# Optimization experiments

Measured on AMD Instinct MI355X. Metric: run time of the kernel, lower is better.

## Reference

```python
import jax, jax.numpy as jnp
import numpy as np

EPS = 1e-5
DG = 8          # deformable groups
KK = 9          # 3x3 taps


def group_norm(x, w, b, G=32, eps=EPS):
    B, C, H, W = x.shape
    xr = x.reshape(B, G, -1)
    m = xr.mean(-1, keepdims=True)
    v = xr.var(-1, keepdims=True)
    xn = ((xr - m) * jax.lax.rsqrt(v + eps)).reshape(B, C, H, W)
    return xn * w[None, :, None, None] + b[None, :, None, None]


def conv1x1(x, w, b):
    return jnp.einsum('bchw,oc->bohw', x, w[:, :, 0, 0]) + b[None, :, None, None]


def conv3x3(x, w, b):
    y = jax.lax.conv_general_dilated(x, w, (1, 1), ((1, 1), (1, 1)),
                                     dimension_numbers=('NCHW', 'OIHW', 'NCHW'))
    return y + b[None, :, None, None]


def bilinear_resize(x, Ho, Wo):
    # matches F.interpolate(mode='bilinear', align_corners=False)
    B, C, H, W = x.shape
    sy = jnp.maximum((jnp.arange(Ho, dtype=x.dtype) + 0.5) * (H / Ho) - 0.5, 0.0)
    sx = jnp.maximum((jnp.arange(Wo, dtype=x.dtype) + 0.5) * (W / Wo) - 0.5, 0.0)
    y0 = jnp.floor(sy).astype(jnp.int32); y1 = jnp.minimum(y0 + 1, H - 1)
    x0 = jnp.floor(sx).astype(jnp.int32); x1 = jnp.minimum(x0 + 1, W - 1)
    fy = (sy - y0)[None, None, :, None]
    fx = (sx - x0)[None, None, None, :]
    v00 = x[:, :, y0][:, :, :, x0]; v01 = x[:, :, y0][:, :, :, x1]
    v10 = x[:, :, y1][:, :, :, x0]; v11 = x[:, :, y1][:, :, :, x1]
    return (v00 * (1 - fy) * (1 - fx) + v01 * (1 - fy) * fx
            + v10 * fy * (1 - fx) + v11 * fy * fx)


def modulated_deform_conv(x, offset, mask, w, b, G=DG):
    # x: [B,C,H,W]; offset: [B,2*G*9,H,W]; mask: [B,G*9,H,W]; w: [Co,C,3,3]
    B, C, H, W = x.shape
    Cg = C // G
    Co = w.shape[0]
    off = offset.reshape(B, G, 2 * KK, H, W)
    oy = off[:, :, 0::2]   # [B,G,9,H,W]
    ox = off[:, :, 1::2]
    m = mask.reshape(B, G, KK, H, W)
    kh, kw = jnp.meshgrid(jnp.arange(3), jnp.arange(3), indexing='ij')
    kh = kh.reshape(KK).astype(x.dtype); kw = kw.reshape(KK).astype(x.dtype)
    hh = jnp.arange(H, dtype=x.dtype); ww = jnp.arange(W, dtype=x.dtype)
    # sampling positions: p = p0 + p_k + offset   (stride 1, pad 1, dil 1)
    py = oy + (hh[None, None, None, :, None] - 1.0 + kh[None, None, :, None, None])
    px = ox + (ww[None, None, None, None, :] - 1.0 + kw[None, None, :, None, None])
    xf = x.reshape(B, G, Cg, H * W)
    wr = w.reshape(Co, G, Cg, KK)
    y0 = jnp.floor(py); x0 = jnp.floor(px)
    out = jnp.zeros((B, Co, H, W), x.dtype)
    for dy in (0.0, 1.0):
        for dx in (0.0, 1.0):
            yi = y0 + dy; xi = x0 + dx
            wgt = (1.0 - jnp.abs(py - yi)) * (1.0 - jnp.abs(px - xi))
            valid = (yi >= 0) & (yi < H) & (xi >= 0) & (xi < W)
            wgt = wgt * valid.astype(x.dtype)
            idx = (jnp.clip(yi, 0, H - 1) * W + jnp.clip(xi, 0, W - 1)).astype(jnp.int32)
            g = jnp.take_along_axis(xf, idx.reshape(B, G, 1, KK * H * W), axis=3)
            g = g.reshape(B, G, Cg, KK, H, W)
            out = out + jnp.einsum('bgckhw,bgkhw,ogck->bohw', g, wgt * m, wr)
    return out + b[None, :, None, None]


def setup_inputs() -> dict:
    key = jax.random.key(0)
    ks = jax.random.split(key, 12)
    C = 256
    B, H, W = 2, 96, 96
    s = lambda fan: 1.0 / np.sqrt(fan)
    inp = {
        'feat_l': jax.random.normal(ks[0], (B, C, H, W), jnp.float32),
        'feat_s': jax.random.normal(ks[1], (B, C, H // 2, W // 2), jnp.float32),
        # FeatureSelectionModule params
        'fsm_atten_w': jax.random.normal(ks[2], (C, C, 1, 1), jnp.float32) * s(C),
        'fsm_atten_b': jnp.zeros((C,), jnp.float32),
        'fsm_gn1_w': jnp.ones((C,), jnp.float32),
        'fsm_gn1_b': jnp.zeros((C,), jnp.float32),
        'fsm_conv_w': jax.random.normal(ks[3], (C, C, 1, 1), jnp.float32) * s(C),
        'fsm_conv_b': jnp.zeros((C,), jnp.float32),
        'fsm_gn2_w': jnp.ones((C,), jnp.float32),
        'fsm_gn2_b': jnp.zeros((C,), jnp.float32),
        # offset 1x1 conv (in 2C -> C) + GN
        'off_w': jax.random.normal(ks[4], (C, 2 * C, 1, 1), jnp.float32) * s(2 * C),
        'off_b': jnp.zeros((C,), jnp.float32),
        'gn_off_w': jnp.ones((C,), jnp.float32),
        'gn_off_b': jnp.zeros((C,), jnp.float32),
        # dcn_v2: conv_offset_mask (C -> 8*3*9=216, k=3) and main 3x3 weight
        'com_w': jax.random.normal(ks[5], (DG * 3 * KK, C, 3, 3), jnp.float32) * s(C * 9),
        'com_b': jnp.zeros((DG * 3 * KK,), jnp.float32),
        'dcn_w': jax.random.normal(ks[6], (C, C, 3, 3), jnp.float32) * s(C * 9),
        'dcn_b': jnp.zeros((C,), jnp.float32),
    }
    return inp


def reference(feat_l, feat_s, fsm_atten_w, fsm_atten_b, fsm_gn1_w, fsm_gn1_b,
              fsm_conv_w, fsm_conv_b, fsm_gn2_w, fsm_gn2_b,
              off_w, off_b, gn_off_w, gn_off_b, com_w, com_b, dcn_w, dcn_b):
    B, C, H, W = feat_l.shape
    feat_up = bilinear_resize(feat_s, H, W)
    # FeatureSelectionModule
    pooled = feat_l.mean(axis=(2, 3), keepdims=True)  # avg_pool over full spatial
    atten = jax.nn.sigmoid(group_norm(conv1x1(pooled, fsm_atten_w, fsm_atten_b),
                                      fsm_gn1_w, fsm_gn1_b))
    x = feat_l + feat_l * atten
    feat_arm = group_norm(conv1x1(x, fsm_conv_w, fsm_conv_b), fsm_gn2_w, fsm_gn2_b)
    # offset feature
    cat = jnp.concatenate([feat_arm, feat_up * 2.0], axis=1)
    offset_feat = group_norm(conv1x1(cat, off_w, off_b), gn_off_w, gn_off_b)
    # dcn_v2 with extra_offset_mask=True
    om = conv3x3(offset_feat, com_w, com_b)              # [B, 216, H, W]
    o1, o2, msk = jnp.split(om, 3, axis=1)
    offset = jnp.concatenate([o1, o2], axis=1)           # [B, 144, H, W]
    mask = jax.nn.sigmoid(msk)                           # [B, 72, H, W]
    d = modulated_deform_conv(feat_up, offset, mask, dcn_w, dcn_b)
    return jax.nn.relu(d) + feat_arm
```

## Files before the change

### kernel.cpp

```cpp
#include <hip/hip_runtime.h>

constexpr int B_ = 2, C_ = 256, H_ = 96, W_ = 96, HW_ = H_ * W_;
constexpr int Hs_ = 48, Ws_ = 48;
constexpr int OMC_ = 216;
constexpr int GNG_ = 32;

typedef __attribute__((ext_vector_type(8))) short short8;
typedef __attribute__((ext_vector_type(16))) float f32x16;

__global__ __launch_bounds__(256) void k_pool(const float* __restrict__ x, float* __restrict__ pooled) {
    int bc = blockIdx.x;
    const float* p = x + (size_t)bc * HW_;
    float s = 0.f;
    for (int i = threadIdx.x; i < HW_; i += 256) s += p[i];
    __shared__ float red[256];
    red[threadIdx.x] = s; __syncthreads();
    for (int o = 128; o > 0; o >>= 1) {
        if (threadIdx.x < o) red[threadIdx.x] += red[threadIdx.x + o];
        __syncthreads();
    }
    if (threadIdx.x == 0) pooled[bc] = red[0] * (1.f / (float)HW_);
}

__global__ __launch_bounds__(256) void k_atten(const float* __restrict__ pooled,
                                               const float* __restrict__ aw, const float* __restrict__ ab,
                                               const float* __restrict__ g1w, const float* __restrict__ g1b,
                                               float* __restrict__ atten) {
    int b = blockIdx.x;
    __shared__ float pl[C_];
    __shared__ float av[C_];
    int o = threadIdx.x;
    pl[o] = pooled[b * C_ + o];
    __syncthreads();
    float s = ab[o];
    const float* wr = aw + (size_t)o * C_;
    for (int c = 0; c < C_; ++c) s += wr[c] * pl[c];
    av[o] = s; __syncthreads();
    int g = o >> 3;
    float m = 0.f;
    for (int i = 0; i < 8; ++i) m += av[g * 8 + i];
    m *= 0.125f;
    float v = 0.f;
    for (int i = 0; i < 8; ++i) { float d = av[g * 8 + i] - m; v += d * d; }
    v *= 0.125f;
    float xn = (s - m) * rsqrtf(v + 1e-5f);
    float gn = xn * g1w[o] + g1b[o];
    atten[b * C_ + o] = 1.f + 1.f / (1.f + expf(-gn));
}

__global__ __launch_bounds__(256) void k_up(const float* __restrict__ fs, float* __restrict__ up_cf) {
    int bc = blockIdx.x;
    const float* src = fs + (size_t)bc * (Hs_ * Ws_);
    float* dst = up_cf + (size_t)bc * HW_;
    for (int i = threadIdx.x; i < HW_; i += 256) {
        int y = i / W_, x = i - y * W_;
        float syf = fmaxf((y + 0.5f) * 0.5f - 0.5f, 0.f);
        float sxf = fmaxf((x + 0.5f) * 0.5f - 0.5f, 0.f);
        int y0 = (int)syf, x0 = (int)sxf;
        int y1 = min(y0 + 1, Hs_ - 1), x1 = min(x0 + 1, Ws_ - 1);
        float fy = syf - (float)y0, fx = sxf - (float)x0;
        float v00 = src[y0 * Ws_ + x0], v01 = src[y0 * Ws_ + x1];
        float v10 = src[y1 * Ws_ + x0], v11 = src[y1 * Ws_ + x1];
        dst[i] = v00 * (1.f - fy) * (1.f - fx) + v01 * (1.f - fy) * fx
               + v10 * fy * (1.f - fx) + v11 * fy * fx;
    }
}

__global__ __launch_bounds__(256) void k_transpose(const float* __restrict__ src, float* __restrict__ dst) {
    __shared__ float t[32][33];
    int b = blockIdx.z;
    int c0 = blockIdx.x * 32, p0 = blockIdx.y * 32;
    const float* s = src + (size_t)b * C_ * HW_;
    float* d = dst + (size_t)b * HW_ * C_;
    int tx = threadIdx.x & 31, ty = threadIdx.x >> 5;
    for (int i = 0; i < 32; i += 8)
        t[ty + i][tx] = s[(size_t)(c0 + ty + i) * HW_ + p0 + tx];
    __syncthreads();
    for (int i = 0; i < 32; i += 8)
        d[(size_t)(p0 + ty + i) * C_ + c0 + tx] = t[tx][ty + i];
}

__global__ void k_gnfin(float* stats, float inv_count) {
    int t = threadIdx.x;
    float s = stats[t * 2], q = stats[t * 2 + 1];
    float mean = s * inv_count;
    float var = q * inv_count - mean * mean;
    stats[t * 2] = mean;
    stats[t * 2 + 1] = rsqrtf(var + 1e-5f);
}

__global__ __launch_bounds__(256) void k_gnapply(float* __restrict__ buf, const float* __restrict__ stats,
                                                 const float* __restrict__ w, const float* __restrict__ bgn) {
    int bc = blockIdx.x; int b = bc / C_; int c = bc - b * C_; int g = c >> 3;
    float mean = stats[(b * GNG_ + g) * 2], rstd = stats[(b * GNG_ + g) * 2 + 1];
    float sw = w[c] * rstd;
    float sb = bgn[c] - mean * sw;
    float* p = buf + (size_t)bc * HW_;
    for (int i = threadIdx.x; i < HW_; i += 256) p[i] = p[i] * sw + sb;
}

__device__ __forceinline__ void bf16split(float v, ushort& h, ushort& l) {
    unsigned u = __float_as_uint(v);
    unsigned hr = (u + 0x7FFFu + ((u >> 16) & 1u)) >> 16;
    float hf = __uint_as_float(hr << 16);
    unsigned u2 = __float_as_uint(v - hf);
    unsigned lr_ = (u2 + 0x7FFFu + ((u2 >> 16) & 1u)) >> 16;
    h = (ushort)hr; l = (ushort)lr_;
}

__global__ __launch_bounds__(256) void k_prepw(const float* __restrict__ w,
                                               ushort* __restrict__ ah, ushort* __restrict__ al) {
    int q = blockIdx.x;
    int m = threadIdx.x;
    int tap = q >> 3, cb = q & 7;
    ushort hbuf[32], lbuf[32];
    #pragma unroll
    for (int kk = 0; kk < 32; ++kk) {
        float v = 0.f;
        if (m < OMC_) v = w[((size_t)m * 256 + cb * 32 + kk) * 9 + tap];
        bf16split(v, hbuf[kk], lbuf[kk]);
    }
    size_t base = ((size_t)q * 256 + m) * 32;
    #pragma unroll
    for (int i = 0; i < 4; ++i) {
        ((uint4*)(ah + base))[i] = ((const uint4*)hbuf)[i];
        ((uint4*)(al + base))[i] = ((const uint4*)lbuf)[i];
    }
}

__global__ __launch_bounds__(256) void k_prepdw(const float* __restrict__ w,
                                                ushort* __restrict__ dh, ushort* __restrict__ dl) {
    int q = blockIdx.x;
    int m = threadIdx.x;
    int g = q / 9, k = q - g * 9;
    ushort hbuf[32], lbuf[32];
    #pragma unroll
    for (int kk = 0; kk < 32; ++kk) {
        float v = w[((size_t)m * 256 + g * 32 + kk) * 9 + k];
        bf16split(v, hbuf[kk], lbuf[kk]);
    }
    size_t base = ((size_t)q * 256 + m) * 32;
    #pragma unroll
    for (int i = 0; i < 4; ++i) {
        ((uint4*)(dh + base))[i] = ((const uint4*)hbuf)[i];
        ((uint4*)(dl + base))[i] = ((const uint4*)lbuf)[i];
    }
}

__global__ __launch_bounds__(256) void k_prepcw(const float* __restrict__ w, int K,
                                                ushort* __restrict__ h, ushort* __restrict__ l) {
    int q = blockIdx.x;
    int m = threadIdx.x;
    ushort hbuf[32], lbuf[32];
    #pragma unroll
    for (int kk = 0; kk < 32; ++kk) {
        float v = w[(size_t)m * K + q * 32 + kk];
        bf16split(v, hbuf[kk], lbuf[kk]);
    }
    size_t base = ((size_t)q * 256 + m) * 32;
    #pragma unroll
    for (int i = 0; i < 4; ++i) {
        ((uint4*)(h + base))[i] = ((const uint4*)hbuf)[i];
        ((uint4*)(l + base))[i] = ((const uint4*)lbuf)[i];
    }
}

__global__ __launch_bounds__(256) void k_prepxs(const float* __restrict__ src,
                                                ushort* __restrict__ xhh, ushort* __restrict__ xll,
                                                const float* __restrict__ chscale, float cscale) {
    int pt = blockIdx.x;
    int cb = blockIdx.y;
    int b  = blockIdx.z;
    int p0 = pt * 64;
    __shared__ __align__(16) ushort th[32][72];
    __shared__ __align__(16) ushort tl[32][72];
    int t = threadIdx.x;
    int c = t >> 3, j8 = (t & 7) * 8;
    float sc = cscale;
    if (chscale) sc *= chscale[b * 256 + cb * 32 + c];
    const float* srow = src + ((size_t)b * 256 + cb * 32 + c) * HW_ + p0 + j8;
    float4 v0 = *(const float4*)srow;
    float4 v1 = *(const float4*)(srow + 4);
    float vv[8] = {v0.x, v0.y, v0.z, v0.w, v1.x, v1.y, v1.z, v1.w};
    ushort hv[8], lv[8];
    #pragma unroll
    for (int i = 0; i < 8; ++i) bf16split(vv[i] * sc, hv[i], lv[i]);
    *(uint4*)&th[c][j8] = *(const uint4*)hv;
    *(uint4*)&tl[c][j8] = *(const uint4*)lv;
    __syncthreads();
    int p = t >> 2, ch = (t & 3) * 8;
    ushort oh[8], ol[8];
    #pragma unroll
    for (int i = 0; i < 8; ++i) { oh[i] = th[ch + i][p]; ol[i] = tl[ch + i][p]; }
    size_t obase = (((size_t)(b * 8 + cb)) * HW_ + p0 + p) * 32 + ch;
    *(uint4*)(xhh + obase) = *(const uint4*)oh;
    *(uint4*)(xll + obase) = *(const uint4*)ol;
}

__global__ __launch_bounds__(256) void k_prepxg(const float* __restrict__ src,
                                                const float* __restrict__ stats,
                                                const float* __restrict__ gw, const float* __restrict__ gb,
                                                ushort* __restrict__ xhh, ushort* __restrict__ xll) {
    int pt = blockIdx.x;
    int cb = blockIdx.y;
    int b  = blockIdx.z;
    int p0 = pt * 64;
    __shared__ __align__(16) ushort th[32][72];
    __shared__ __align__(16) ushort tl[32][72];
    int t = threadIdx.x;
    int c = t >> 3, j8 = (t & 7) * 8;
    int chg = cb * 32 + c;
    int g = chg >> 3;
    float mean = stats[(b * GNG_ + g) * 2], rstd = stats[(b * GNG_ + g) * 2 + 1];
    float sw = gw[chg] * rstd;
    float sb = gb[chg] - mean * sw;
    const float* srow = src + ((size_t)b * 256 + chg) * HW_ + p0 + j8;
    float4 v0 = *(const float4*)srow;
    float4 v1 = *(const float4*)(srow + 4);
    float vv[8] = {v0.x, v0.y, v0.z, v0.w, v1.x, v1.y, v1.z, v1.w};
    ushort hv[8], lv[8];
    #pragma unroll
    for (int i = 0; i < 8; ++i) bf16split(vv[i] * sw + sb, hv[i], lv[i]);
    *(uint4*)&th[c][j8] = *(const uint4*)hv;
    *(uint4*)&tl[c][j8] = *(const uint4*)lv;
    __syncthreads();
    int p = t >> 2, ch = (t & 3) * 8;
    ushort oh[8], ol[8];
    #pragma unroll
    for (int i = 0; i < 8; ++i) { oh[i] = th[ch + i][p]; ol[i] = tl[ch + i][p]; }
    size_t obase = (((size_t)(b * 8 + cb)) * HW_ + p0 + p) * 32 + ch;
    *(uint4*)(xhh + obase) = *(const uint4*)oh;
    *(uint4*)(xll + obase) = *(const uint4*)ol;
}

__global__ __launch_bounds__(256) void k_conv1x1m(const ushort* __restrict__ wh, const ushort* __restrict__ wl,
                                                  const ushort* __restrict__ xh, const ushort* __restrict__ xl,
                                                  const float* __restrict__ bias, const float* __restrict__ addin,
                                                  float* __restrict__ out, float* __restrict__ stats) {
    int nb = blockIdx.x;
    int mb = blockIdx.y;
    int b  = blockIdx.z;
    int n0 = nb * 64;
    __shared__ __align__(16) ushort Ah[128 * 32];
    __shared__ __align__(16) ushort Al[128 * 32];
    __shared__ __align__(16) ushort Bh[64 * 32];
    __shared__ __align__(16) ushort Bl[64 * 32];
    __shared__ float gsum[16], gsq[16];
    int tid = threadIdx.x;
    if (tid < 16) { gsum[tid] = 0.f; gsq[tid] = 0.f; }
    int lane = tid & 63, wv = tid >> 6;
    int mh = (wv >> 1) * 64;
    int nq = (wv & 1) * 32;
    int lr = lane & 31;
    int kg = lane >> 5;

    f32x16 acc[2] = {};
    int sn = tid >> 2, sch = tid & 3;

    for (int q = 0; q < 8; ++q) {
        const uint4* gah = (const uint4*)(wh + ((size_t)q * 256 + mb * 128) * 32);
        const uint4* gal = (const uint4*)(wl + ((size_t)q * 256 + mb * 128) * 32);
        uint4* sah = (uint4*)Ah; uint4* sal = (uint4*)Al;
        #pragma unroll
        for (int i = 0; i < 2; ++i) {
            int ci = i * 256 + tid;
            int m = ci >> 2, c4 = ci & 3;
            int sw = c4 ^ ((m >> 1) & 3);
            sah[m * 4 + sw] = gah[ci];
            sal[m * 4 + sw] = gal[ci];
        }
        {
            size_t sidx = (((size_t)(b * 8 + q)) * HW_ + n0 + sn) * 32 + sch * 8;
            uint4 vh = *(const uint4*)(xh + sidx);
            uint4 vl = *(const uint4*)(xl + sidx);
            int sw = sch ^ ((sn >> 1) & 3);
            ((uint4*)Bh)[sn * 4 + sw] = vh;
            ((uint4*)Bl)[sn * 4 + sw] = vl;
        }
        __syncthreads();
        #pragma unroll
        for (int s = 0; s < 2; ++s) {
            int chnk = 2 * s + kg;
            int nn = nq + lr;
            int bby = nn * 64 + ((chnk ^ ((nn >> 1) & 3)) << 4);
            short8 bh = *(const short8*)((const char*)Bh + bby);
            short8 bl = *(const short8*)((const char*)Bl + bby);
            #pragma unroll
            for (int f = 0; f < 2; ++f) {
                int row = mh + f * 32 + lr;
                int aby = row * 64 + ((chnk ^ ((row >> 1) & 3)) << 4);
                short8 a_h = *(const short8*)((const char*)Ah + aby);
                short8 a_l = *(const short8*)((const char*)Al + aby);
                acc[f] = __builtin_amdgcn_mfma_f32_32x32x16_bf16(a_h, bh, acc[f], 0, 0, 0);
                acc[f] = __builtin_amdgcn_mfma_f32_32x32x16_bf16(a_h, bl, acc[f], 0, 0, 0);
                acc[f] = __builtin_amdgcn_mfma_f32_32x32x16_bf16(a_l, bh, acc[f], 0, 0, 0);
            }
        }
        __syncthreads();
    }
    int pix = n0 + nq + lr;
    size_t obase = ((size_t)b * 256 + mb * 128) * HW_;
    #pragma unroll
    for (int f = 0; f < 2; ++f) {
        #pragma unroll
        for (int r2 = 0; r2 < 4; ++r2) {
            float qs = 0.f, qq = 0.f;
            #pragma unroll
            for (int r3 = 0; r3 < 4; ++r3) {
                int ml = mh + f * 32 + 8 * r2 + 4 * kg + r3;
                size_t oi = obase + (size_t)ml * HW_ + pix;
                float base = addin ? addin[oi] : bias[mb * 128 + ml];
                float v = acc[f][r2 * 4 + r3] + base;
                out[oi] = v;
                qs += v; qq += v * v;
            }
            if (stats) {
                int gl = (mh >> 3) + f * 4 + r2;
                atomicAdd(&gsum[gl], qs);
                atomicAdd(&gsq[gl], qq);
            }
        }
    }
    __syncthreads();
    if (stats && tid < 16) {
        atomicAdd(&stats[((size_t)b * GNG_ + mb * 16 + tid) * 2 + 0], gsum[tid]);
        atomicAdd(&stats[((size_t)b * GNG_ + mb * 16 + tid) * 2 + 1], gsq[tid]);
    }
}

__global__ __launch_bounds__(256) void k_conv3x3m(const ushort* __restrict__ awt_h, const ushort* __restrict__ awt_l,
                                                  const ushort* __restrict__ xh, const ushort* __restrict__ xl,
                                                  const float* __restrict__ bias,
                                                  float* __restrict__ om1, float* __restrict__ om2) {
    int nb = blockIdx.x;
    int ks = blockIdx.y;
    int b  = blockIdx.z;
    int n0 = nb * 64;
    __shared__ __align__(16) ushort Ah[256 * 32];
    __shared__ __align__(16) ushort Al[256 * 32];
    __shared__ __align__(16) ushort Bh[64 * 32];
    __shared__ __align__(16) ushort Bl[64 * 32];
    int tid = threadIdx.x;
    int lane = tid & 63, wv = tid >> 6;
    int mh = (wv >> 1) * 128;
    int nq = (wv & 1) * 32;
    int lr = lane & 31;
    int kg = lane >> 5;

    f32x16 acc[4] = {};

    int sn = tid >> 2, sch = tid & 3;
    int sp = n0 + sn;
    int spy = sp / W_, spx = sp - spy * W_;

    for (int q = ks * 36; q < ks * 36 + 36; ++q) {
        int tap = q >> 3, cb = q & 7;
        int dy = tap / 3 - 1, dx = tap % 3 - 1;
        const uint4* gah = (const uint4*)(awt_h + (size_t)q * 8192);
        const uint4* gal = (const uint4*)(awt_l + (size_t)q * 8192);
        uint4* sah = (uint4*)Ah; uint4* sal = (uint4*)Al;
        #pragma unroll
        for (int i = 0; i < 4; ++i) {
            int ci = i * 256 + tid;
            int m = ci >> 2, c4 = ci & 3;
            int sw = c4 ^ ((m >> 1) & 3);
            sah[m * 4 + sw] = gah[ci];
            sal[m * 4 + sw] = gal[ci];
        }
        {
            int y = spy + dy, x = spx + dx;
            uint4 vh = {0u, 0u, 0u, 0u}, vl = {0u, 0u, 0u, 0u};
            if ((unsigned)y < (unsigned)H_ && (unsigned)x < (unsigned)W_) {
                size_t sidx = (((size_t)(b * 8 + cb)) * HW_ + y * W_ + x) * 32 + sch * 8;
                vh = *(const uint4*)(xh + sidx);
                vl = *(const uint4*)(xl + sidx);
            }
            int sw = sch ^ ((sn >> 1) & 3);
            ((uint4*)Bh)[sn * 4 + sw] = vh;
            ((uint4*)Bl)[sn * 4 + sw] = vl;
        }
        __syncthreads();
        #pragma unroll
        for (int s = 0; s < 2; ++s) {
            int chnk = 2 * s + kg;
            int nn = nq + lr;
            int bby = nn * 64 + ((chnk ^ ((nn >> 1) & 3)) << 4);
            short8 bh = *(const short8*)((const char*)Bh + bby);
            short8 bl = *(const short8*)((const char*)Bl + bby);
            #pragma unroll
            for (int f = 0; f < 4; ++f) {
                int row = mh + f * 32 + lr;
                int aby = row * 64 + ((chnk ^ ((row >> 1) & 3)) << 4);
                short8 a_h = *(const short8*)((const char*)Ah + aby);
                short8 a_l = *(const short8*)((const char*)Al + aby);
                acc[f] = __builtin_amdgcn_mfma_f32_32x32x16_bf16(a_h, bh, acc[f], 0, 0, 0);
                acc[f] = __builtin_amdgcn_mfma_f32_32x32x16_bf16(a_h, bl, acc[f], 0, 0, 0);
                acc[f] = __builtin_amdgcn_mfma_f32_32x32x16_bf16(a_l, bh, acc[f], 0, 0, 0);
            }
        }
        __syncthreads();
    }
    float* outp = (ks ? om2 : om1) + (size_t)b * OMC_ * HW_;
    int pix = n0 + nq + lr;
    #pragma unroll
    for (int f = 0; f < 4; ++f) {
        #pragma unroll
        for (int r = 0; r < 16; ++r) {
            int m = mh + f * 32 + (r & 3) + 8 * (r >> 2) + 4 * kg;
            if (m < OMC_) {
                float v = acc[f][r] + (ks ? 0.f : bias[m]);
                outp[(size_t)m * HW_ + pix] = v;
            }
        }
    }
}

__global__ __launch_bounds__(256) void k_dcnm(const float* __restrict__ up_cl,
                                              const float* __restrict__ om1, const float* __restrict__ om2,
                                              const ushort* __restrict__ dwh, const ushort* __restrict__ dwl,
                                              const float* __restrict__ dcnb, const float* __restrict__ arm,
                                              float* __restrict__ outp) {
    int nb = blockIdx.x;
    int mb = blockIdx.y;
    int b  = blockIdx.z;
    int n0 = nb * 64;
    __shared__ __align__(16) ushort Ah[128 * 32];
    __shared__ __align__(16) ushort Al[128 * 32];
    __shared__ __align__(16) ushort Bh[64 * 32];
    __shared__ __align__(16) ushort Bl[64 * 32];
    __shared__ float w4s[64][4];
    __shared__ int   yxs[64];
    int tid = threadIdx.x;
    int lane = tid & 63, wv = tid >> 6;
    int mh = (wv >> 1) * 64;
    int nq = (wv & 1) * 32;
    int lr = lane & 31;
    int kg = lane >> 5;

    f32x16 acc[2] = {};

    int sn = tid >> 2, sch = tid & 3;
    const float* upb = up_cl + (size_t)b * HW_ * 256;

    for (int q = 0; q < 72; ++q) {
        int g = q / 9, k = q - g * 9;
        const uint4* gah = (const uint4*)(dwh + ((size_t)q * 256 + mb * 128) * 32);
        const uint4* gal = (const uint4*)(dwl + ((size_t)q * 256 + mb * 128) * 32);
        uint4* sah = (uint4*)Ah; uint4* sal = (uint4*)Al;
        #pragma unroll
        for (int i = 0; i < 2; ++i) {
            int ci = i * 256 + tid;
            int m = ci >> 2, c4 = ci & 3;
            int sw = c4 ^ ((m >> 1) & 3);
            sah[m * 4 + sw] = gah[ci];
            sal[m * 4 + sw] = gal[ci];
        }
        if (tid < 64) {
            int pix = n0 + tid;
            int hh = pix / W_, ww = pix - hh * W_;
            size_t i_oy = ((size_t)b * OMC_ + g * 18 + 2 * k) * HW_ + pix;
            size_t i_mv = ((size_t)b * OMC_ + 144 + g * 9 + k) * HW_ + pix;
            float oy = om1[i_oy] + om2[i_oy];
            float ox = om1[i_oy + HW_] + om2[i_oy + HW_];
            float mv = om1[i_mv] + om2[i_mv];
            float m = 1.f / (1.f + expf(-mv));
            float pyf = oy + (float)(hh - 1 + k / 3);
            float pxf = ox + (float)(ww - 1 + k % 3);
            float y0f = floorf(pyf), x0f = floorf(pxf);
            int y0 = (int)y0f, x0 = (int)x0f;
            float fy = pyf - y0f, fx = pxf - x0f;
            float wy0 = (y0 >= 0 && y0 < H_) ? (1.f - fy) : 0.f;
            float wy1 = (y0 + 1 >= 0 && y0 + 1 < H_) ? fy : 0.f;
            float wx0 = (x0 >= 0 && x0 < W_) ? (1.f - fx) : 0.f;
            float wx1 = (x0 + 1 >= 0 && x0 + 1 < W_) ? fx : 0.f;
            w4s[tid][0] = wy0 * wx0 * m; w4s[tid][1] = wy0 * wx1 * m;
            w4s[tid][2] = wy1 * wx0 * m; w4s[tid][3] = wy1 * wx1 * m;
            yxs[tid] = (y0 << 16) | (x0 & 0xFFFF);
        }
        __syncthreads();
        {
            float4 wv4 = *(const float4*)w4s[sn];
            int yx = yxs[sn];
            int y0 = yx >> 16;
            int x0 = (int)(short)(yx & 0xFFFF);
            int y0c = min(max(y0, 0), H_ - 1), y1c = min(max(y0 + 1, 0), H_ - 1);
            int x0c = min(max(x0, 0), W_ - 1), x1c = min(max(x0 + 1, 0), W_ - 1);
            size_t chof = (size_t)g * 32 + sch * 8;
            const float* p00 = upb + (size_t)(y0c * W_ + x0c) * 256 + chof;
            const float* p01 = upb + (size_t)(y0c * W_ + x1c) * 256 + chof;
            const float* p10 = upb + (size_t)(y1c * W_ + x0c) * 256 + chof;
            const float* p11 = upb + (size_t)(y1c * W_ + x1c) * 256 + chof;
            ushort hv[8], lv[8];
            #pragma unroll
            for (int h2 = 0; h2 < 2; ++h2) {
                float4 t00 = *(const float4*)(p00 + h2 * 4);
                float4 t01 = *(const float4*)(p01 + h2 * 4);
                float4 t10 = *(const float4*)(p10 + h2 * 4);
                float4 t11 = *(const float4*)(p11 + h2 * 4);
                float v0 = wv4.x * t00.x + wv4.y * t01.x + wv4.z * t10.x + wv4.w * t11.x;
                float v1 = wv4.x * t00.y + wv4.y * t01.y + wv4.z * t10.y + wv4.w * t11.y;
                float v2 = wv4.x * t00.z + wv4.y * t01.z + wv4.z * t10.z + wv4.w * t11.z;
                float v3 = wv4.x * t00.w + wv4.y * t01.w + wv4.z * t10.w + wv4.w * t11.w;
                bf16split(v0, hv[h2 * 4 + 0], lv[h2 * 4 + 0]);
                bf16split(v1, hv[h2 * 4 + 1], lv[h2 * 4 + 1]);
                bf16split(v2, hv[h2 * 4 + 2], lv[h2 * 4 + 2]);
                bf16split(v3, hv[h2 * 4 + 3], lv[h2 * 4 + 3]);
            }
            int sw = sch ^ ((sn >> 1) & 3);
            ((uint4*)Bh)[sn * 4 + sw] = *(const uint4*)hv;
            ((uint4*)Bl)[sn * 4 + sw] = *(const uint4*)lv;
        }
        __syncthreads();
        #pragma unroll
        for (int s = 0; s < 2; ++s) {
            int chnk = 2 * s + kg;
            int nn = nq + lr;
            int bby = nn * 64 + ((chnk ^ ((nn >> 1) & 3)) << 4);
            short8 bh = *(const short8*)((const char*)Bh + bby);
            short8 bl = *(const short8*)((const char*)Bl + bby);
            #pragma unroll
            for (int f = 0; f < 2; ++f) {
                int row = mh + f * 32 + lr;
                int aby = row * 64 + ((chnk ^ ((row >> 1) & 3)) << 4);
                short8 a_h = *(const short8*)((const char*)Ah + aby);
                short8 a_l = *(const short8*)((const char*)Al + aby);
                acc[f] = __builtin_amdgcn_mfma_f32_32x32x16_bf16(a_h, bh, acc[f], 0, 0, 0);
                acc[f] = __builtin_amdgcn_mfma_f32_32x32x16_bf16(a_h, bl, acc[f], 0, 0, 0);
                acc[f] = __builtin_amdgcn_mfma_f32_32x32x16_bf16(a_l, bh, acc[f], 0, 0, 0);
            }
        }
        __syncthreads();
    }
    int pix = n0 + nq + lr;
    #pragma unroll
    for (int f = 0; f < 2; ++f) {
        #pragma unroll
        for (int r = 0; r < 16; ++r) {
            int m = mb * 128 + mh + f * 32 + (r & 3) + 8 * (r >> 2) + 4 * kg;
            float v = acc[f][r] + dcnb[m];
            v = fmaxf(v, 0.f) + arm[((size_t)b * 256 + m) * HW_ + pix];
            outp[((size_t)b * 256 + m) * HW_ + pix] = v;
        }
    }
}

extern "C" void kernel_launch(void* const* d_in, const int* in_sizes, int n_in,
                              void* d_out, int out_size, void* d_ws, size_t ws_size,
                              hipStream_t stream) {
    const float* feat_l = (const float*)d_in[0];
    const float* feat_s = (const float*)d_in[1];
    const float* aw  = (const float*)d_in[2];
    const float* ab  = (const float*)d_in[3];
    const float* g1w = (const float*)d_in[4];
    const float* g1b = (const float*)d_in[5];
    const float* cw  = (const float*)d_in[6];
    const float* cb  = (const float*)d_in[7];
    const float* g2w = (const float*)d_in[8];
    const float* g2b = (const float*)d_in[9];
    const float* ow  = (const float*)d_in[10];
    const float* ob  = (const float*)d_in[11];
    const float* gow = (const float*)d_in[12];
    const float* gob = (const float*)d_in[13];
    const float* comw= (const float*)d_in[14];
    const float* comb= (const float*)d_in[15];
    const float* dcnw= (const float*)d_in[16];
    const float* dcnb= (const float*)d_in[17];
    float* out = (float*)d_out;
    float* ws = (float*)d_ws;

    size_t off = 0;
    float* up_cf = ws + off; off += (size_t)B_ * C_ * HW_;
    float* up_cl = ws + off; off += (size_t)B_ * C_ * HW_;
    float* arm   = ws + off; off += (size_t)B_ * C_ * HW_;
    float* offf  = ws + off; off += (size_t)B_ * C_ * HW_;
    float* wtreg = ws + off; off += (size_t)2304 * 256;
    float* xreg  = ws + off; off += (size_t)B_ * 8 * HW_ * 32;
    float* pooled= ws + off; off += B_ * C_;
    float* atten = ws + off; off += B_ * C_;
    float* stats = ws + off; off += 4 * B_ * GNG_;
    float* stats_arm = stats;
    float* stats_off = stats + 2 * B_ * GNG_;

    ushort* c1h = (ushort*)wtreg;
    ushort* c1l = c1h + (size_t)8 * 256 * 32;
    ushort* c2h = c1l + (size_t)8 * 256 * 32;
    ushort* c2l = c2h + (size_t)16 * 256 * 32;
    ushort* awth = (ushort*)wtreg;
    ushort* awtl = awth + (size_t)72 * 256 * 32;
    ushort* dwh  = (ushort*)wtreg;
    ushort* dwl  = dwh + (size_t)72 * 256 * 32;

    ushort* xh = (ushort*)xreg;
    ushort* xl = xh + (size_t)B_ * 8 * HW_ * 32;

    float* om1 = offf;
    float* om2 = up_cf;

    hipMemsetAsync(stats, 0, 4 * B_ * GNG_ * sizeof(float), stream);
    k_pool<<<B_ * C_, 256, 0, stream>>>(feat_l, pooled);
    k_atten<<<B_, 256, 0, stream>>>(pooled, aw, ab, g1w, g1b, atten);
    k_up<<<B_ * C_, 256, 0, stream>>>(feat_s, up_cf);
    k_transpose<<<dim3(8, 288, B_), 256, 0, stream>>>(up_cf, up_cl);

    k_prepcw<<<8, 256, 0, stream>>>(cw, 256, c1h, c1l);
    k_prepxs<<<dim3(144, 8, B_), 256, 0, stream>>>(feat_l, xh, xl, atten, 1.f);
    k_conv1x1m<<<dim3(144, 2, B_), 256, 0, stream>>>(c1h, c1l, xh, xl, cb, nullptr, arm, stats_arm);
    k_gnfin<<<1, 64, 0, stream>>>(stats_arm, 1.f / (8.f * HW_));
    k_gnapply<<<B_ * C_, 256, 0, stream>>>(arm, stats_arm, g2w, g2b);

    k_prepcw<<<16, 256, 0, stream>>>(ow, 512, c2h, c2l);
    k_prepxs<<<dim3(144, 8, B_), 256, 0, stream>>>(arm, xh, xl, nullptr, 1.f);
    k_conv1x1m<<<dim3(144, 2, B_), 256, 0, stream>>>(c2h, c2l, xh, xl, ob, nullptr, offf, nullptr);
    k_prepxs<<<dim3(144, 8, B_), 256, 0, stream>>>(up_cf, xh, xl, nullptr, 2.f);
    k_conv1x1m<<<dim3(144, 2, B_), 256, 0, stream>>>(c2h + (size_t)8 * 256 * 32, c2l + (size_t)8 * 256 * 32,
                                                     xh, xl, ob, offf, offf, stats_off);
    k_gnfin<<<1, 64, 0, stream>>>(stats_off, 1.f / (8.f * HW_));

    k_prepw<<<72, 256, 0, stream>>>(comw, awth, awtl);
    k_prepxg<<<dim3(144, 8, B_), 256, 0, stream>>>(offf, stats_off, gow, gob, xh, xl);
    k_conv3x3m<<<dim3(144, 2, B_), 256, 0, stream>>>(awth, awtl, xh, xl, comb, om1, om2);

    k_prepdw<<<72, 256, 0, stream>>>(dcnw, dwh, dwl);
    k_dcnm<<<dim3(144, 2, B_), 256, 0, stream>>>(up_cl, om1, om2, dwh, dwl, dcnb, arm, out);
}
```

Measured before the change: 561.0 us.

## Split DCN reduction over two K halves and register-prefetch next tap's gathers

The deformable conv GEMM's 72-tap reduction is split into two halves run by separate blocks, doubling the grid. Partial sums go to the output and a scratch buffer, and a new combine kernel adds them with bias, ReLU and the residual. Inside the loop, each thread now computes its own sampling weights and gathers the next tap's corners and weight tile into registers while the current tap's MFMAs run. This replaces the shared-memory handoff and one barrier, aiming to hide gather latency. The cost is higher register pressure, extra partial-sum traffic and an additional kernel launch.

```diff
diff --git a/kernel.cpp b/kernel.cpp
--- a/kernel.cpp
+++ b/kernel.cpp
@@ -415,21 +415,58 @@
     }
 }
 
+struct GState {
+    float4 w4;
+    float4 t00a, t01a, t10a, t11a, t00b, t01b, t10b, t11b;
+};
+
+__device__ __forceinline__ void corner_gather(int q, int b, int pix, int hh, int ww, int sch,
+                                              const float* __restrict__ om1, const float* __restrict__ om2,
+                                              const float* __restrict__ upb, GState& st) {
+    int g = q / 9, k = q - g * 9;
+    size_t i_oy = ((size_t)b * OMC_ + g * 18 + 2 * k) * HW_ + pix;
+    size_t i_mv = ((size_t)b * OMC_ + 144 + g * 9 + k) * HW_ + pix;
+    float oy = om1[i_oy] + om2[i_oy];
+    float ox = om1[i_oy + HW_] + om2[i_oy + HW_];
+    float mv = om1[i_mv] + om2[i_mv];
+    float m = 1.f / (1.f + expf(-mv));
+    float pyf = oy + (float)(hh - 1 + k / 3);
+    float pxf = ox + (float)(ww - 1 + k % 3);
+    float y0f = floorf(pyf), x0f = floorf(pxf);
+    int y0 = (int)y0f, x0 = (int)x0f;
+    float fy = pyf - y0f, fx = pxf - x0f;
+    float wy0 = (y0 >= 0 && y0 < H_) ? (1.f - fy) : 0.f;
+    float wy1 = (y0 + 1 >= 0 && y0 + 1 < H_) ? fy : 0.f;
+    float wx0 = (x0 >= 0 && x0 < W_) ? (1.f - fx) : 0.f;
+    float wx1 = (x0 + 1 >= 0 && x0 + 1 < W_) ? fx : 0.f;
+    st.w4.x = wy0 * wx0 * m; st.w4.y = wy0 * wx1 * m;
+    st.w4.z = wy1 * wx0 * m; st.w4.w = wy1 * wx1 * m;
+    int y0c = min(max(y0, 0), H_ - 1), y1c = min(max(y0 + 1, 0), H_ - 1);
+    int x0c = min(max(x0, 0), W_ - 1), x1c = min(max(x0 + 1, 0), W_ - 1);
+    size_t chof = (size_t)g * 32 + sch * 8;
+    const float* p00 = upb + (size_t)(y0c * W_ + x0c) * 256 + chof;
+    const float* p01 = upb + (size_t)(y0c * W_ + x1c) * 256 + chof;
+    const float* p10 = upb + (size_t)(y1c * W_ + x0c) * 256 + chof;
+    const float* p11 = upb + (size_t)(y1c * W_ + x1c) * 256 + chof;
+    st.t00a = *(const float4*)p00; st.t00b = *(const float4*)(p00 + 4);
+    st.t01a = *(const float4*)p01; st.t01b = *(const float4*)(p01 + 4);
+    st.t10a = *(const float4*)p10; st.t10b = *(const float4*)(p10 + 4);
+    st.t11a = *(const float4*)p11; st.t11b = *(const float4*)(p11 + 4);
+}
+
 __global__ __launch_bounds__(256) void k_dcnm(const float* __restrict__ up_cl,
                                               const float* __restrict__ om1, const float* __restrict__ om2,
                                               const ushort* __restrict__ dwh, const ushort* __restrict__ dwl,
-                                              const float* __restrict__ dcnb, const float* __restrict__ arm,
-                                              float* __restrict__ outp) {
+                                              float* __restrict__ out0, float* __restrict__ pacc) {
     int nb = blockIdx.x;
-    int mb = blockIdx.y;
+    int mb = blockIdx.y & 1;
+    int ks = blockIdx.y >> 1;
     int b  = blockIdx.z;
     int n0 = nb * 64;
     __shared__ __align__(16) ushort Ah[128 * 32];
     __shared__ __align__(16) ushort Al[128 * 32];
     __shared__ __align__(16) ushort Bh[64 * 32];
     __shared__ __align__(16) ushort Bl[64 * 32];
-    __shared__ float w4s[64][4];
-    __shared__ int   yxs[64];
     int tid = threadIdx.x;
     int lane = tid & 63, wv = tid >> 6;
     int mh = (wv >> 1) * 64;
@@ -438,77 +475,62 @@
     int kg = lane >> 5;
 
     f32x16 acc[2] = {};
-
     int sn = tid >> 2, sch = tid & 3;
     const float* upb = up_cl + (size_t)b * HW_ * 256;
 
-    for (int q = 0; q < 72; ++q) {
-        int g = q / 9, k = q - g * 9;
-        const uint4* gah = (const uint4*)(dwh + ((size_t)q * 256 + mb * 128) * 32);
-        const uint4* gal = (const uint4*)(dwl + ((size_t)q * 256 + mb * 128) * 32);
-        uint4* sah = (uint4*)Ah; uint4* sal = (uint4*)Al;
-        #pragma unroll
-        for (int i = 0; i < 2; ++i) {
-            int ci = i * 256 + tid;
-            int m = ci >> 2, c4 = ci & 3;
-            int sw = c4 ^ ((m >> 1) & 3);
-            sah[m * 4 + sw] = gah[ci];
-            sal[m * 4 + sw] = gal[ci];
-        }
-        if (tid < 64) {
-            int pix = n0 + tid;
-            int hh = pix / W_, ww = pix - hh * W_;
-            size_t i_oy = ((size_t)b * OMC_ + g * 18 + 2 * k) * HW_ + pix;
-            size_t i_mv = ((size_t)b * OMC_ + 144 + g * 9 + k) * HW_ + pix;
-            float oy = om1[i_oy] + om2[i_oy];
-            float ox = om1[i_oy + HW_] + om2[i_oy + HW_];
-            float mv = om1[i_mv] + om2[i_mv];
-            float m = 1.f / (1.f + expf(-mv));
-            float pyf = oy + (float)(hh - 1 + k / 3);
-            float pxf = ox + (float)(ww - 1 + k % 3);
-            float y0f = floorf(pyf), x0f = floorf(pxf);
-            int y0 = (int)y0f, x0 = (int)x0f;
-            float fy = pyf - y0f, fx = pxf - x0f;
-            float wy0 = (y0 >= 0 && y0 < H_) ? (1.f - fy) : 0.f;
-            float wy1 = (y0 + 1 >= 0 && y0 + 1 < H_) ? fy : 0.f;
-            float wx0 = (x0 >= 0 && x0 < W_) ? (1.f - fx) : 0.f;
-            float wx1 = (x0 + 1 >= 0 && x0 + 1 < W_) ? fx : 0.f;
-            w4s[tid][0] = wy0 * wx0 * m; w4s[tid][1] = wy0 * wx1 * m;
-            w4s[tid][2] = wy1 * wx0 * m; w4s[tid][3] = wy1 * wx1 * m;
-            yxs[tid] = (y0 << 16) | (x0 & 0xFFFF);
-        }
-        __syncthreads();
+    int pix = n0 + sn;
+    int hh = pix / W_, ww = pix - hh * W_;
+    int q0 = ks * 36;
+
+    GState st;
+    uint4 aH0, aH1, aL0, aL1;
+    {
+        const uint4* gah = (const uint4*)(dwh + ((size_t)q0 * 256 + mb * 128) * 32);
+        const uint4* gal = (const uint4*)(dwl + ((size_t)q0 * 256 + mb * 128) * 32);
+        aH0 = gah[tid]; aH1 = gah[256 + tid];
+        aL0 = gal[tid]; aL1 = gal[256 + tid];
+        corner_gather(q0, b, pix, hh, ww, sch, om1, om2, upb, st);
+    }
+
+    for (int qi = 0; qi < 36; ++qi) {
+        int q = q0 + qi;
+        ushort hv[8], lv[8];
         {
-            float4 wv4 = *(const float4*)w4s[sn];
-            int yx = yxs[sn];
-            int y0 = yx >> 16;
-            int x0 = (int)(short)(yx & 0xFFFF);
-            int y0c = min(max(y0, 0), H_ - 1), y1c = min(max(y0 + 1, 0), H_ - 1);
-            int x0c = min(max(x0, 0), W_ - 1), x1c = min(max(x0 + 1, 0), W_ - 1);
-            size_t chof = (size_t)g * 32 + sch * 8;
-            const float* p00 = upb + (size_t)(y0c * W_ + x0c) * 256 + chof;
-            const float* p01 = upb + (size_t)(y0c * W_ + x1c) * 256 + chof;
-            const float* p10 = upb + (size_t)(y1c * W_ + x0c) * 256 + chof;
-            const float* p11 = upb + (size_t)(y1c * W_ + x1c) * 256 + chof;
-            ushort hv[8], lv[8];
-            #pragma unroll
-            for (int h2 = 0; h2 < 2; ++h2) {
-                float4 t00 = *(const float4*)(p00 + h2 * 4);
-                float4 t01 = *(const float4*)(p01 + h2 * 4);
-                float4 t10 = *(const float4*)(p10 + h2 * 4);
-                float4 t11 = *(const float4*)(p11 + h2 * 4);
-                float v0 = wv4.x * t00.x + wv4.y * t01.x + wv4.z * t10.x + wv4.w * t11.x;
-                float v1 = wv4.x * t00.y + wv4.y * t01.y + wv4.z * t10.y + wv4.w * t11.y;
-                float v2 = wv4.x * t00.z + wv4.y * t01.z + wv4.z * t10.z + wv4.w * t11.z;
-                float v3 = wv4.x * t00.w + wv4.y * t01.w + wv4.z * t10.w + wv4.w * t11.w;
-                bf16split(v0, hv[h2 * 4 + 0], lv[h2 * 4 + 0]);
-                bf16split(v1, hv[h2 * 4 + 1], lv[h2 * 4 + 1]);
-                bf16split(v2, hv[h2 * 4 + 2], lv[h2 * 4 + 2]);
-                bf16split(v3, hv[h2 * 4 + 3], lv[h2 * 4 + 3]);
-            }
-            int sw = sch ^ ((sn >> 1) & 3);
-            ((uint4*)Bh)[sn * 4 + sw] = *(const uint4*)hv;
-            ((uint4*)Bl)[sn * 4 + sw] = *(const uint4*)lv;
+            float4 w4 = st.w4;
+            float v0 = w4.x * st.t00a.x + w4.y * st.t01a.x + w4.z * st.t10a.x + w4.w * st.t11a.x;
+            float v1 = w4.x * st.t00a.y + w4.y * st.t01a.y + w4.z * st.t10a.y + w4.w * st.t11a.y;
+            float v2 = w4.x * st.t00a.z + w4.y * st.t01a.z + w4.z * st.t10a.z + w4.w * st.t11a.z;
+            float v3 = w4.x * st.t00a.w + w4.y * st.t01a.w + w4.z * st.t10a.w + w4.w * st.t11a.w;
+            float v4 = w4.x * st.t00b.x + w4.y * st.t01b.x + w4.z * st.t10b.x + w4.w * st.t11b.x;
+            float v5 = w4.x * st.t00b.y + w4.y * st.t01b.y + w4.z * st.t10b.y + w4.w * st.t11b.y;
+            float v6 = w4.x * st.t00b.z + w4.y * st.t01b.z + w4.z * st.t10b.z + w4.w * st.t11b.z;
+            float v7 = w4.x * st.t00b.w + w4.y * st.t01b.w + w4.z * st.t10b.w + w4.w * st.t11b.w;
+            bf16split(v0, hv[0], lv[0]); bf16split(v1, hv[1], lv[1]);
+            bf16split(v2, hv[2], lv[2]); bf16split(v3, hv[3], lv[3]);
+            bf16split(v4, hv[4], lv[4]); bf16split(v5, hv[5], lv[5]);
+            bf16split(v6, hv[6], lv[6]); bf16split(v7, hv[7], lv[7]);
+        }
+        __syncthreads();
+        {
+            uint4* sah = (uint4*)Ah; uint4* sal = (uint4*)Al;
+            int m0i = tid >> 2, c40 = tid & 3;
+            int sw0 = c40 ^ ((m0i >> 1) & 3);
+            sah[m0i * 4 + sw0] = aH0; sal[m0i * 4 + sw0] = aL0;
+            int ci1 = 256 + tid;
+            int m1i = ci1 >> 2, c41 = ci1 & 3;
+            int sw1 = c41 ^ ((m1i >> 1) & 3);
+            sah[m1i * 4 + sw1] = aH1; sal[m1i * 4 + sw1] = aL1;
+            int swb = sch ^ ((sn >> 1) & 3);
+            ((uint4*)Bh)[sn * 4 + swb] = *(const uint4*)hv;
+            ((uint4*)Bl)[sn * 4 + swb] = *(const uint4*)lv;
+        }
+        if (qi + 1 < 36) {
+            int qn = q + 1;
+            const uint4* gah = (const uint4*)(dwh + ((size_t)qn * 256 + mb * 128) * 32);
+            const uint4* gal = (const uint4*)(dwl + ((size_t)qn * 256 + mb * 128) * 32);
+            aH0 = gah[tid]; aH1 = gah[256 + tid];
+            aL0 = gal[tid]; aL1 = gal[256 + tid];
+            corner_gather(qn, b, pix, hh, ww, sch, om1, om2, upb, st);
         }
         __syncthreads();
         #pragma unroll
@@ -531,16 +553,36 @@
         }
         __syncthreads();
     }
-    int pix = n0 + nq + lr;
+    int pixe = n0 + nq + lr;
+    float* dst = (ks ? pacc : out0);
     #pragma unroll
     for (int f = 0; f < 2; ++f) {
         #pragma unroll
         for (int r = 0; r < 16; ++r) {
             int m = mb * 128 + mh + f * 32 + (r & 3) + 8 * (r >> 2) + 4 * kg;
-            float v = acc[f][r] + dcnb[m];
-            v = fmaxf(v, 0.f) + arm[((size_t)b * 256 + m) * HW_ + pix];
-            outp[((size_t)b * 256 + m) * HW_ + pix] = v;
-        }
+            dst[((size_t)b * 256 + m) * HW_ + pixe] = acc[f][r];
+        }
+    }
+}
+
+__global__ __launch_bounds__(256) void k_dcncomb(float* __restrict__ out, const float* __restrict__ pacc,
+                                                 const float* __restrict__ dcnb, const float* __restrict__ arm) {
+    int bc = blockIdx.x;
+    int c = bc & 255;
+    float bi = dcnb[c];
+    size_t base = (size_t)bc * HW_;
+    const float4* pp = (const float4*)(pacc + base);
+    const float4* ap = (const float4*)(arm + base);
+    float4* op = (float4*)(out + base);
+    for (int i = threadIdx.x; i < HW_ / 4; i += 256) {
+        float4 o = op[i];
+        float4 p = pp[i];
+        float4 a = ap[i];
+        o.x = fmaxf(o.x + p.x + bi, 0.f) + a.x;
+        o.y = fmaxf(o.y + p.y + bi, 0.f) + a.y;
+        o.z = fmaxf(o.z + p.z + bi, 0.f) + a.z;
+        o.w = fmaxf(o.w + p.w + bi, 0.f) + a.w;
+        op[i] = o;
     }
 }
 
@@ -592,6 +634,7 @@
 
     ushort* xh = (ushort*)xreg;
     ushort* xl = xh + (size_t)B_ * 8 * HW_ * 32;
+    float* pacc = xreg;
 
     float* om1 = offf;
     float* om2 = up_cf;
@@ -621,5 +664,6 @@
     k_conv3x3m<<<dim3(144, 2, B_), 256, 0, stream>>>(awth, awtl, xh, xl, comb, om1, om2);
 
     k_prepdw<<<72, 256, 0, stream>>>(dcnw, dwh, dwl);
-    k_dcnm<<<dim3(144, 2, B_), 256, 0, stream>>>(up_cl, om1, om2, dwh, dwl, dcnb, arm, out);
-}
+    k_dcnm<<<dim3(144, 4, B_), 256, 0, stream>>>(up_cl, om1, om2, dwh, dwl, out, pacc);
+    k_dcncomb<<<B_ * C_, 256, 0, stream>>>(out, pacc, dcnb, arm);
+}
```

Result: faster. 544.1 us (-3.0%).
